# Kernel tuning notes

Measured on AMD Instinct MI355X. Metric: run time of the kernel, lower is better.

Reference implementation:

```python
import jax, jax.numpy as jnp
import numpy as np

B, N, K = 16, 8192, 16
H1, H3 = 512, 64
EPS = 1e-5


def _bn(x, g, b):
    # BatchNorm1d training-mode math: normalize per-channel (last axis) over all other axes.
    ax = tuple(range(x.ndim - 1))
    m = x.mean(ax, keepdims=True)
    v = x.var(ax, keepdims=True)  # biased variance, as in torch BN forward
    return (x - m) * jax.lax.rsqrt(v + EPS) * g + b


def _gather(h, idx):
    # h: [b,n,f], idx: [b,n,k] -> [b,n,k,f] per-batch neighbor gather
    return jax.vmap(lambda hb, ib: hb[ib])(h, idx)


def _forward(data, knn, e1_w, e1_b, e1_g, e1_be,
             gc1_w, gc1_b, g1_g, g1_be, gc2_w, gc2_b, g2_g, g2_be,
             e2_w, e2_b, e2_g, e2_be,
             d1_w, d1_b, d1_g, d1_be, d2_w, d2_b, d2_g, d2_be):
    b, n, _ = data.shape
    # local covariance features
    neigh = _gather(data, knn)                       # [b,n,K,3]
    cen = neigh - neigh.mean(axis=2, keepdims=True)
    cov = jnp.einsum('bnki,bnkj->bnij', cen, cen) / (K - 1)
    x = jnp.concatenate([data, cov.reshape(b, n, 9)], axis=-1)  # [b,n,12]
    # e_layers1: Linear(12,h3) + BN + ReLU
    x = jax.nn.relu(_bn(x @ e1_w + e1_b, e1_g, e1_be))
    # GCNConv over uniform-degree kNN graph with self loop: (h_i + sum_j h_j)/(K+1)
    deg = float(K + 1)
    h = x @ gc1_w
    h = (h + _gather(h, knn).sum(axis=2)) / deg + gc1_b
    x = jax.nn.relu(_bn(h, g1_g, g1_be))
    h = x @ gc2_w
    h = (h + _gather(h, knn).sum(axis=2)) / deg + gc2_b
    x = jax.nn.relu(_bn(h, g2_g, g2_be))             # [b,n,h1]
    # AdaptiveMaxPool1d(1) over nodes
    x = x.max(axis=1, keepdims=True)                 # [b,1,h1]
    # e_layers2: Linear(h1,h1) + BN + ReLU
    x = jax.nn.relu(_bn(x @ e2_w + e2_b, e2_g, e2_be))
    # decode: folding grid
    nx_ = int(1 + (n * 120 / 60) ** 0.5)
    ny_ = int(1 + (n * 60 / 120) ** 0.5)
    xg = jnp.linspace(1.0, 120.0, nx_)
    yg = jnp.linspace(1.0, 60.0, ny_)
    grid = jnp.stack(jnp.meshgrid(xg, yg, indexing='ij'), axis=-1).reshape(-1, 2)[:n]
    kfeat = jnp.broadcast_to(x, (b, n, x.shape[-1]))  # codeword repeated per node
    y = jnp.broadcast_to(grid[None], (b, n, 2))
    z = jnp.concatenate([kfeat, y], axis=-1)          # [b,n,h1+2]
    z = jax.nn.relu(_bn(z @ d1_w + d1_b, d1_g, d1_be))
    z = jnp.concatenate([kfeat, z], axis=-1)          # [b,n,h1+3]
    z = jax.nn.relu(_bn(z @ d2_w + d2_b, d2_g, d2_be))
    return z                                          # [b,n,3]


def setup_inputs() -> dict:
    key = jax.random.key(0)
    ks = jax.random.split(key, 8)

    def lin(k, i, o):
        s = 1.0 / np.sqrt(i)
        return jax.random.uniform(k, (i, o), jnp.float32, -s, s)

    ones = lambda c: jnp.ones((c,), jnp.float32)
    zeros = lambda c: jnp.zeros((c,), jnp.float32)
    return {
        'data': jax.random.normal(ks[0], (B, N, 3), jnp.float32),
        'knn': jax.random.randint(ks[1], (B, N, K), 0, N),
        'e1_w': lin(ks[2], 12, H3), 'e1_b': zeros(H3), 'e1_g': ones(H3), 'e1_be': zeros(H3),
        'gc1_w': lin(ks[3], H3, 2 * H3), 'gc1_b': zeros(2 * H3), 'g1_g': ones(2 * H3), 'g1_be': zeros(2 * H3),
        'gc2_w': lin(ks[4], 2 * H3, H1), 'gc2_b': zeros(H1), 'g2_g': ones(H1), 'g2_be': zeros(H1),
        'e2_w': lin(ks[5], H1, H1), 'e2_b': zeros(H1), 'e2_g': ones(H1), 'e2_be': zeros(H1),
        'd1_w': lin(ks[6], H1 + 2, 3), 'd1_b': zeros(3), 'd1_g': ones(3), 'd1_be': zeros(3),
        'd2_w': lin(ks[7], H1 + 3, 3), 'd2_b': zeros(3), 'd2_g': ones(3), 'd2_be': zeros(3),
    }


def reference(data, knn, e1_w, e1_b, e1_g, e1_be,
              gc1_w, gc1_b, g1_g, g1_be, gc2_w, gc2_b, g2_g, g2_be,
              e2_w, e2_b, e2_g, e2_be,
              d1_w, d1_b, d1_g, d1_be, d2_w, d2_b, d2_g, d2_be):
    return _forward(data, knn, e1_w, e1_b, e1_g, e1_be,
                    gc1_w, gc1_b, g1_g, g1_be, gc2_w, gc2_b, g2_g, g2_be,
                    e2_w, e2_b, e2_g, e2_be,
                    d1_w, d1_b, d1_g, d1_be, d2_w, d2_b, d2_g, d2_be)
```

## Files before the change

kernel.cpp:

```cpp
#include <hip/hip_runtime.h>
#include <hip/hip_fp16.h>
#include <stdint.h>

#define BATCH 16
#define NPTS  8192
#define KNN   16
#define NROWS (BATCH*NPTS)
#define EPSBN 1e-5f
#define DEGINV (1.0f/17.0f)

typedef _Float16 f16x8 __attribute__((ext_vector_type(8)));
typedef float    f32x4 __attribute__((ext_vector_type(4)));

__device__ __forceinline__ unsigned short f2hu(float f) {
    union { _Float16 h; unsigned short u; } cv;
    cv.h = (_Float16)f;
    return cv.u;
}
__device__ __forceinline__ float hu2f(unsigned short u) {
    union { unsigned short u; _Float16 h; } cv;
    cv.u = u;
    return (float)cv.h;
}
__device__ __forceinline__ unsigned fenc(float f) {
    unsigned u = __float_as_uint(f);
    return (int)u >= 0 ? (u | 0x80000000u) : ~u;
}
__device__ __forceinline__ float fdec(unsigned k) {
    return (k & 0x80000000u) ? __uint_as_float(k & 0x7FFFFFFFu) : __uint_as_float(~k);
}

#define SZ_S1    0
#define SZ_S2P   128
#define SZ_S3P   16512
#define SZ_S4    82048
#define SZ_C1    83072
#define SZ_GN    83080
#define SZ_D2    83088
#define SZ_SCSH1 83096
#define SZ_SCSH2 83224
#define SZ_TOT   83480

__global__ __launch_bounds__(256) void k_prep(
    const float* __restrict__ gc1w, const float* __restrict__ gc2w,
    const float* __restrict__ d1w, const float* __restrict__ d1b,
    unsigned short* __restrict__ W1T, unsigned short* __restrict__ W2T,
    float* __restrict__ gn, float* __restrict__ statszone, unsigned* __restrict__ mm)
{
    int t = blockIdx.x * 256 + threadIdx.x;
    int NT_ = gridDim.x * 256;
    for (int i = t; i < 65536; i += NT_) {
        int c = i >> 7, k = i & 127;
        W2T[i] = f2hu(gc2w[k * 512 + c]);
    }
    for (int i = t; i < 8192; i += NT_) {
        int c = i >> 6, k = i & 63;
        W1T[i] = f2hu(gc1w[k * 128 + c]);
    }
    for (int i = t; i < SZ_TOT; i += NT_) statszone[i] = 0.f;
    for (int i = t; i < 8192; i += NT_) mm[i] = 0u;
    for (int i = t; i < 8192; i += NT_) mm[8192 + i] = 0xFFFFFFFFu;
    for (int n = t; n < 8192; n += NT_) {
        int ix = n / 65, iy = n % 65;
        float gx = 1.f + ix * (119.f / 128.f);
        float gy = 1.f + iy * (59.f / 64.f);
        #pragma unroll
        for (int j = 0; j < 3; j++)
            gn[n * 3 + j] = gx * d1w[512 * 3 + j] + gy * d1w[513 * 3 + j] + d1b[j];
    }
}

__global__ __launch_bounds__(256) void k_cov_e1(
    const float* __restrict__ data, const int* __restrict__ knn,
    const float* __restrict__ e1w, const float* __restrict__ e1b,
    float* __restrict__ a1)
{
    __shared__ float w[12 * 64];
    __shared__ float bias[64];
    int tid = threadIdx.x;
    for (int i = tid; i < 768; i += 256) w[i] = e1w[i];
    if (tid < 64) bias[tid] = e1b[tid];
    __syncthreads();

    int gid = blockIdx.x * 256 + tid;
    int b = gid >> 13;
    const float* db = data + (size_t)b * NPTS * 3;
    const int4* k4 = (const int4*)knn + gid * 4;

    float sx = 0, sy = 0, sz = 0, Sxx = 0, Sxy = 0, Sxz = 0, Syy = 0, Syz = 0, Szz = 0;
    #pragma unroll
    for (int jj = 0; jj < 4; jj++) {
        int4 q = k4[jj];
        int id[4] = {q.x, q.y, q.z, q.w};
        #pragma unroll
        for (int u = 0; u < 4; u++) {
            const float* p = db + (size_t)id[u] * 3;
            float x = p[0], y = p[1], z = p[2];
            sx += x; sy += y; sz += z;
            Sxx += x * x; Sxy += x * y; Sxz += x * z;
            Syy += y * y; Syz += y * z; Szz += z * z;
        }
    }
    float mx = sx * (1.f / 16.f), my = sy * (1.f / 16.f), mz = sz * (1.f / 16.f);
    const float inv15 = 1.f / 15.f;
    float x12[12];
    x12[0] = data[(size_t)gid * 3 + 0];
    x12[1] = data[(size_t)gid * 3 + 1];
    x12[2] = data[(size_t)gid * 3 + 2];
    x12[3] = (Sxx - 16.f * mx * mx) * inv15;
    x12[4] = (Sxy - 16.f * mx * my) * inv15;
    x12[5] = (Sxz - 16.f * mx * mz) * inv15;
    x12[6] = x12[4];
    x12[7] = (Syy - 16.f * my * my) * inv15;
    x12[8] = (Syz - 16.f * my * mz) * inv15;
    x12[9] = x12[5];
    x12[10] = x12[8];
    x12[11] = (Szz - 16.f * mz * mz) * inv15;

    float* arow = a1 + (size_t)gid * 64;
    for (int c0 = 0; c0 < 64; c0 += 4) {
        float4 v;
        float* vv = (float*)&v;
        #pragma unroll
        for (int u = 0; u < 4; u++) {
            int c = c0 + u;
            float acc = bias[c];
            #pragma unroll
            for (int i = 0; i < 12; i++) acc += x12[i] * w[i * 64 + c];
            vv[u] = acc;
        }
        *(float4*)(arow + c0) = v;
    }
}

__global__ __launch_bounds__(256) void k_reduce_a1(
    const float* __restrict__ a1, float* __restrict__ stats1)
{
    int tid = threadIdx.x;
    int c = tid & 63, rq = tid >> 6;
    float s = 0.f, q = 0.f;
    for (int row = blockIdx.x * 4 + rq; row < NROWS; row += gridDim.x * 4) {
        float v = a1[(size_t)row * 64 + c];
        s += v; q += v * v;
    }
    __shared__ float red[2][256];
    red[0][tid] = s; red[1][tid] = q;
    __syncthreads();
    if (tid < 64) {
        s = red[0][tid] + red[0][tid + 64] + red[0][tid + 128] + red[0][tid + 192];
        q = red[1][tid] + red[1][tid + 64] + red[1][tid + 128] + red[1][tid + 192];
        atomicAdd(stats1 + tid, s);
        atomicAdd(stats1 + 64 + tid, q);
    }
}

template <int C, int NPARTS>
__global__ __launch_bounds__(256) void k_bncoef(
    const float* __restrict__ statsIn,
    const float* __restrict__ gamma, const float* __restrict__ beta,
    float* __restrict__ scsh)
{
    int ch = threadIdx.x;
    if (ch < C) {
        float s = 0.f, q = 0.f;
        for (int p = 0; p < NPARTS; p++) {
            s += statsIn[p * 2 * C + ch];
            q += statsIn[p * 2 * C + C + ch];
        }
        float m = s * (1.f / NROWS);
        float var = fmaxf(q * (1.f / NROWS) - m * m, 0.f);
        float sc = gamma[ch] * rsqrtf(var + EPSBN);
        scsh[ch] = sc;
        scsh[C + ch] = beta[ch] - m * sc;
    }
}

template <int CIN>
__global__ __launch_bounds__(256) void k_gather(
    const float* __restrict__ ain, const int* __restrict__ knn,
    const float* __restrict__ scsh, unsigned short* __restrict__ S)
{
    constexpr int GPR = CIN / 4;
    constexpr int R = 256 / GPR;
    constexpr int BPB = NPTS / R;

    __shared__ int nidx[R * KNN];

    int tid = threadIdx.x;
    int blk = blockIdx.x;
    int xcd = blk & 7;
    int idx = blk >> 3;
    int batch = xcd + 8 * (idx / BPB);
    int within = idx % BPB;
    int node0 = batch * NPTS + within * R;

    if (tid < R * KNN / 4) {
        const int4* ksrc = (const int4*)(knn + (size_t)node0 * KNN);
        ((int4*)nidx)[tid] = ksrc[tid];
    }
    __syncthreads();

    int t = tid & (GPR - 1);
    int r = tid / GPR;
    int col4 = t * 4;
    float4 scv = *(const float4*)(scsh + col4);
    float4 shv = *(const float4*)(scsh + CIN + col4);

    int row = node0 + r;
    const float* abase = ain + (size_t)batch * NPTS * CIN;

    float4 v = *(const float4*)(ain + (size_t)row * CIN + col4);
    float a0 = fmaxf(v.x * scv.x + shv.x, 0.f);
    float a1v = fmaxf(v.y * scv.y + shv.y, 0.f);
    float a2v = fmaxf(v.z * scv.z + shv.z, 0.f);
    float a3v = fmaxf(v.w * scv.w + shv.w, 0.f);
    #pragma unroll
    for (int jn = 0; jn < KNN; jn++) {
        int src = nidx[r * KNN + jn];
        float4 wv = *(const float4*)(abase + (size_t)src * CIN + col4);
        a0  += fmaxf(wv.x * scv.x + shv.x, 0.f);
        a1v += fmaxf(wv.y * scv.y + shv.y, 0.f);
        a2v += fmaxf(wv.z * scv.z + shv.z, 0.f);
        a3v += fmaxf(wv.w * scv.w + shv.w, 0.f);
    }
    uint2 o;
    o.x = f2hu(a0)  | ((unsigned)f2hu(a1v) << 16);
    o.y = f2hu(a2v) | ((unsigned)f2hu(a3v) << 16);
    *(uint2*)(S + (size_t)row * CIN + col4) = o;
}

template <int CIN>
__global__ __launch_bounds__(256) void k_gather16(
    const unsigned short* __restrict__ ain, const int* __restrict__ knn,
    const float* __restrict__ scsh, unsigned short* __restrict__ S)
{
    constexpr int GPR = CIN / 8;
    constexpr int R = 256 / GPR;
    constexpr int BPB = NPTS / R;

    __shared__ int nidx[R * KNN];

    int tid = threadIdx.x;
    int blk = blockIdx.x;
    int xcd = blk & 7;
    int idx = blk >> 3;
    int batch = xcd + 8 * (idx / BPB);
    int within = idx % BPB;
    int node0 = batch * NPTS + within * R;

    if (tid < R * KNN / 4) {
        const int4* ksrc = (const int4*)(knn + (size_t)node0 * KNN);
        ((int4*)nidx)[tid] = ksrc[tid];
    }
    __syncthreads();

    int t = tid & (GPR - 1);
    int r = tid / GPR;
    int col8 = t * 8;
    float sc8[8], sh8[8];
    #pragma unroll
    for (int j = 0; j < 8; j++) { sc8[j] = scsh[col8 + j]; sh8[j] = scsh[CIN + col8 + j]; }

    int row = node0 + r;
    const unsigned short* abase = ain + (size_t)batch * NPTS * CIN;

    float acc8[8];
    {
        uint4 v = *(const uint4*)(ain + (size_t)row * CIN + col8);
        unsigned wds[4] = {v.x, v.y, v.z, v.w};
        #pragma unroll
        for (int j = 0; j < 4; j++) {
            acc8[2*j]   = fmaxf(hu2f((unsigned short)(wds[j] & 0xFFFF)) * sc8[2*j]   + sh8[2*j],   0.f);
            acc8[2*j+1] = fmaxf(hu2f((unsigned short)(wds[j] >> 16))    * sc8[2*j+1] + sh8[2*j+1], 0.f);
        }
    }
    #pragma unroll
    for (int jn = 0; jn < KNN; jn++) {
        int src = nidx[r * KNN + jn];
        uint4 v = *(const uint4*)(abase + (size_t)src * CIN + col8);
        unsigned wds[4] = {v.x, v.y, v.z, v.w};
        #pragma unroll
        for (int j = 0; j < 4; j++) {
            acc8[2*j]   += fmaxf(hu2f((unsigned short)(wds[j] & 0xFFFF)) * sc8[2*j]   + sh8[2*j],   0.f);
            acc8[2*j+1] += fmaxf(hu2f((unsigned short)(wds[j] >> 16))    * sc8[2*j+1] + sh8[2*j+1], 0.f);
        }
    }
    uint4 o;
    o.x = f2hu(acc8[0]) | ((unsigned)f2hu(acc8[1]) << 16);
    o.y = f2hu(acc8[2]) | ((unsigned)f2hu(acc8[3]) << 16);
    o.z = f2hu(acc8[4]) | ((unsigned)f2hu(acc8[5]) << 16);
    o.w = f2hu(acc8[6]) | ((unsigned)f2hu(acc8[7]) << 16);
    *(uint4*)(S + (size_t)row * CIN + col8) = o;
}

template <int CIN, int COUT, bool STORE>
__global__ __launch_bounds__(256) void k_gemm(
    const unsigned short* __restrict__ S, const unsigned short* __restrict__ WT,
    const float* __restrict__ bias,
    unsigned short* __restrict__ aout, float* __restrict__ statsOut, unsigned* __restrict__ mm)
{
    constexpr int KC = CIN / 32;
    constexpr int NT = COUT / 64;
    constexpr int NHALF = (NT >= 2) ? 2 : 1;
    constexpr int NTH = NT / NHALF;
    constexpr int MT = 128;
    constexpr int BPB = NPTS / MT;

    int tid = threadIdx.x;
    int blk = blockIdx.x;
    int xcd = blk & 7;
    int idx = blk >> 3;
    int batch = xcd + 8 * (idx / BPB);
    int within = idx % BPB;
    int node0 = batch * NPTS + within * MT;
    int pout = batch * 4 + (within >> 4);

    int lane = tid & 63, wv = tid >> 6;
    int n15 = lane & 15, qd = lane >> 4;
    int c0 = wv * (COUT / 4);

    const unsigned short* Sbase = S + (size_t)node0 * CIN + (size_t)n15 * CIN + qd * 8;

    #pragma unroll
    for (int half = 0; half < NHALF; half++) {
        f16x8 wf[KC][NTH];
        float bz[NTH];
        #pragma unroll
        for (int nth = 0; nth < NTH; nth++) {
            int c = c0 + (half * NTH + nth) * 16 + n15;
            bz[nth] = bias[c];
            #pragma unroll
            for (int kc = 0; kc < KC; kc++)
                wf[kc][nth] = *(const f16x8*)(WT + (size_t)c * CIN + kc * 32 + qd * 8);
        }
        float sA[NTH], qA[NTH], mxA[NTH], mnA[NTH];
        #pragma unroll
        for (int nth = 0; nth < NTH; nth++) {
            sA[nth] = 0.f; qA[nth] = 0.f; mxA[nth] = -3.4e38f; mnA[nth] = 3.4e38f;
        }

        for (int mt = 0; mt < MT / 16; mt++) {
            f16x8 af[KC];
            #pragma unroll
            for (int kc = 0; kc < KC; kc++)
                af[kc] = *(const f16x8*)(Sbase + (size_t)mt * 16 * CIN + kc * 32);

            f32x4 acc[NTH];
            #pragma unroll
            for (int nth = 0; nth < NTH; nth++) acc[nth] = (f32x4)(0.f);
            #pragma unroll
            for (int kc = 0; kc < KC; kc++)
                #pragma unroll
                for (int nth = 0; nth < NTH; nth++)
                    acc[nth] = __builtin_amdgcn_mfma_f32_16x16x32_f16(af[kc], wf[kc][nth], acc[nth], 0, 0, 0);

            #pragma unroll
            for (int nth = 0; nth < NTH; nth++) {
                int c = c0 + (half * NTH + nth) * 16 + n15;
                #pragma unroll
                for (int r = 0; r < 4; r++) {
                    float v = acc[nth][r] * DEGINV + bz[nth];
                    if (STORE) {
                        int node = node0 + mt * 16 + qd * 4 + r;
                        aout[(size_t)node * COUT + c] = f2hu(v);
                    }
                    sA[nth] += v; qA[nth] += v * v;
                    mxA[nth] = fmaxf(mxA[nth], v); mnA[nth] = fminf(mnA[nth], v);
                }
            }
        }

        #pragma unroll
        for (int nth = 0; nth < NTH; nth++) {
            int c = c0 + (half * NTH + nth) * 16 + n15;
            float s = sA[nth], q = qA[nth];
            s += __shfl_xor(s, 16); s += __shfl_xor(s, 32);
            q += __shfl_xor(q, 16); q += __shfl_xor(q, 32);
            if (!STORE) {
                float mx = mxA[nth], mn = mnA[nth];
                mx = fmaxf(mx, __shfl_xor(mx, 16)); mx = fmaxf(mx, __shfl_xor(mx, 32));
                mn = fminf(mn, __shfl_xor(mn, 16)); mn = fminf(mn, __shfl_xor(mn, 32));
                if (lane < 16) {
                    atomicMax(mm + batch * COUT + c, fenc(mx));
                    atomicMin(mm + BATCH * COUT + batch * COUT + c, fenc(mn));
                }
            }
            if (lane < 16) {
                atomicAdd(statsOut + (size_t)pout * 2 * COUT + c, s);
                atomicAdd(statsOut + (size_t)pout * 2 * COUT + COUT + c, q);
            }
        }
    }
}

__global__ __launch_bounds__(256) void k_e2(
    const float* __restrict__ stats3p, const unsigned* __restrict__ mm,
    const float* __restrict__ g2g, const float* __restrict__ g2be,
    const float* __restrict__ e2w, const float* __restrict__ e2b,
    float* __restrict__ a4, float* __restrict__ stats4)
{
    __shared__ float pooled[512];
    int b = blockIdx.x, tid = threadIdx.x;
    for (int c = tid; c < 512; c += 256) {
        float s = 0.f, qq = 0.f;
        for (int p = 0; p < 64; p++) {
            s += stats3p[p * 1024 + c];
            qq += stats3p[p * 1024 + 512 + c];
        }
        float m = s * (1.f / NROWS);
        float var = fmaxf(qq * (1.f / NROWS) - m * m, 0.f);
        float sc = g2g[c] * rsqrtf(var + EPSBN);
        float sh = g2be[c] - m * sc;
        float amax = fdec(mm[b * 512 + c]);
        float amin = fdec(mm[8192 + b * 512 + c]);
        pooled[c] = fmaxf(fmaxf(sc * amax + sh, 0.f), fmaxf(sc * amin + sh, 0.f));
    }
    __syncthreads();
    int ca = tid, cb = tid + 256;
    float acc1 = e2b[ca], acc2 = e2b[cb];
    for (int f = 0; f < 512; f++) {
        float pv = pooled[f];
        acc1 += pv * e2w[f * 512 + ca];
        acc2 += pv * e2w[f * 512 + cb];
    }
    a4[b * 512 + ca] = acc1; a4[b * 512 + cb] = acc2;
    atomicAdd(stats4 + ca, acc1); atomicAdd(stats4 + 512 + ca, acc1 * acc1);
    atomicAdd(stats4 + cb, acc2); atomicAdd(stats4 + 512 + cb, acc2 * acc2);
}

__global__ __launch_bounds__(256) void k_code(
    const float* __restrict__ a4, const float* __restrict__ stats4,
    const float* __restrict__ e2g, const float* __restrict__ e2be,
    const float* __restrict__ d1w, const float* __restrict__ d2w,
    const float* __restrict__ gn,
    float* __restrict__ c1, float* __restrict__ c2,
    float* __restrict__ c1stats, float* __restrict__ gnstats)
{
    int b = blockIdx.x, tid = threadIdx.x;
    int lane = tid & 63, wv = tid >> 6;
    float p1[3] = {0, 0, 0}, p2[3] = {0, 0, 0};
    for (int c = tid; c < 512; c += 256) {
        float s = stats4[c], qq = stats4[512 + c];
        float m = s * (1.f / 16.f);
        float var = fmaxf(qq * (1.f / 16.f) - m * m, 0.f);
        float sc = e2g[c] * rsqrtf(var + EPSBN);
        float sh = e2be[c] - m * sc;
        float cv = fmaxf(sc * a4[b * 512 + c] + sh, 0.f);
        #pragma unroll
        for (int j = 0; j < 3; j++) {
            p1[j] += cv * d1w[c * 3 + j];
            p2[j] += cv * d2w[c * 3 + j];
        }
    }
    __shared__ float red[4][6];
    #pragma unroll
    for (int j = 0; j < 3; j++)
        for (int off = 32; off; off >>= 1) {
            p1[j] += __shfl_xor(p1[j], off);
            p2[j] += __shfl_xor(p2[j], off);
        }
    if (lane == 0) {
        #pragma unroll
        for (int j = 0; j < 3; j++) { red[wv][j] = p1[j]; red[wv][3 + j] = p2[j]; }
    }
    __syncthreads();
    if (tid < 3) {
        float v = red[0][tid] + red[1][tid] + red[2][tid] + red[3][tid];
        c1[b * 3 + tid] = v;
        atomicAdd(c1stats + tid, v);
        atomicAdd(c1stats + 3 + tid, v * v);
    } else if (tid < 6) {
        int j = tid - 3;
        float v = red[0][tid] + red[1][tid] + red[2][tid] + red[3][tid];
        c2[b * 3 + j] = v;
    }
    if (blockIdx.x == 0) {
        float g1[3] = {0, 0, 0}, g2s[3] = {0, 0, 0};
        for (int n = tid; n < NPTS; n += 256) {
            #pragma unroll
            for (int j = 0; j < 3; j++) {
                float g = gn[n * 3 + j];
                g1[j] += g; g2s[j] += g * g;
            }
        }
        #pragma unroll
        for (int j = 0; j < 3; j++)
            for (int off = 32; off; off >>= 1) {
                g1[j] += __shfl_xor(g1[j], off);
                g2s[j] += __shfl_xor(g2s[j], off);
            }
        __shared__ float redg[4][6];
        if (lane == 0) {
            #pragma unroll
            for (int j = 0; j < 3; j++) { redg[wv][j] = g1[j]; redg[wv][3 + j] = g2s[j]; }
        }
        __syncthreads();
        if (tid < 6)
            gnstats[tid] = redg[0][tid] + redg[1][tid] + redg[2][tid] + redg[3][tid];
    }
}

__device__ __forceinline__ void d1_coefs(
    const float* c1stats, const float* gnstats,
    const float* d1g, const float* d1be, float* scd, float* shd)
{
    #pragma unroll
    for (int j = 0; j < 3; j++) {
        float mc = c1stats[j] * (1.f / 16.f), qc = c1stats[3 + j] * (1.f / 16.f);
        float mg = gnstats[j] * (1.f / 8192.f), qg = gnstats[3 + j] * (1.f / 8192.f);
        float m = mc + mg;
        float var = fmaxf((qc - mc * mc) + (qg - mg * mg), 0.f);
        float sc = d1g[j] * rsqrtf(var + EPSBN);
        scd[j] = sc;
        shd[j] = d1be[j] - m * sc;
    }
}

__global__ __launch_bounds__(256) void k_d2stats(
    const float* __restrict__ c1, const float* __restrict__ c2, const float* __restrict__ gn,
    const float* __restrict__ c1stats, const float* __restrict__ gnstats,
    const float* __restrict__ d1g, const float* __restrict__ d1be,
    const float* __restrict__ d2w, const float* __restrict__ d2b,
    float* __restrict__ statsd2)
{
    int gid = blockIdx.x * 256 + threadIdx.x;
    int b = gid >> 13, n = gid & 8191;
    int lane = threadIdx.x & 63, wv = threadIdx.x >> 6;
    float scd[3], shd[3];
    d1_coefs(c1stats, gnstats, d1g, d1be, scd, shd);
    float z3[3];
    #pragma unroll
    for (int j = 0; j < 3; j++)
        z3[j] = fmaxf(scd[j] * (c1[b * 3 + j] + gn[n * 3 + j]) + shd[j], 0.f);
    float vals[6];
    #pragma unroll
    for (int u = 0; u < 3; u++) {
        float a = c2[b * 3 + u]
                + z3[0] * d2w[512 * 3 + u]
                + z3[1] * d2w[513 * 3 + u]
                + z3[2] * d2w[514 * 3 + u]
                + d2b[u];
        vals[u] = a; vals[3 + u] = a * a;
    }
    #pragma unroll
    for (int j = 0; j < 6; j++)
        for (int off = 32; off; off >>= 1) vals[j] += __shfl_xor(vals[j], off);
    __shared__ float red[4][6];
    if (lane == 0) {
        #pragma unroll
        for (int j = 0; j < 6; j++) red[wv][j] = vals[j];
    }
    __syncthreads();
    if (threadIdx.x < 6)
        atomicAdd(statsd2 + threadIdx.x,
                  red[0][threadIdx.x] + red[1][threadIdx.x] + red[2][threadIdx.x] + red[3][threadIdx.x]);
}

__global__ __launch_bounds__(256) void k_out(
    const float* __restrict__ c1, const float* __restrict__ c2, const float* __restrict__ gn,
    const float* __restrict__ c1stats, const float* __restrict__ gnstats,
    const float* __restrict__ statsd2,
    const float* __restrict__ d1g, const float* __restrict__ d1be,
    const float* __restrict__ d2w, const float* __restrict__ d2b,
    const float* __restrict__ d2g, const float* __restrict__ d2be,
    float* __restrict__ out)
{
    int gid = blockIdx.x * 256 + threadIdx.x;
    int b = gid >> 13, n = gid & 8191;
    float scd[3], shd[3];
    d1_coefs(c1stats, gnstats, d1g, d1be, scd, shd);
    float z3[3];
    #pragma unroll
    for (int j = 0; j < 3; j++)
        z3[j] = fmaxf(scd[j] * (c1[b * 3 + j] + gn[n * 3 + j]) + shd[j], 0.f);
    #pragma unroll
    for (int u = 0; u < 3; u++) {
        float a = c2[b * 3 + u]
                + z3[0] * d2w[512 * 3 + u]
                + z3[1] * d2w[513 * 3 + u]
                + z3[2] * d2w[514 * 3 + u]
                + d2b[u];
        float m2 = statsd2[u] * (1.f / (float)NROWS);
        float v2 = fmaxf(statsd2[3 + u] * (1.f / (float)NROWS) - m2 * m2, 0.f);
        float sc = d2g[u] * rsqrtf(v2 + EPSBN);
        float sh = d2be[u] - m2 * sc;
        out[(size_t)gid * 3 + u] = fmaxf(sc * a + sh, 0.f);
    }
}

extern "C" void kernel_launch(void* const* d_in, const int* in_sizes, int n_in,
                              void* d_out, int out_size, void* d_ws, size_t ws_size,
                              hipStream_t stream)
{
    (void)in_sizes; (void)n_in; (void)out_size; (void)ws_size;
    const float* data = (const float*)d_in[0];
    const int*   knn  = (const int*)d_in[1];
    const float* e1w = (const float*)d_in[2],  *e1b = (const float*)d_in[3];
    const float* e1g = (const float*)d_in[4],  *e1be = (const float*)d_in[5];
    const float* gc1w = (const float*)d_in[6], *gc1b = (const float*)d_in[7];
    const float* g1g = (const float*)d_in[8],  *g1be = (const float*)d_in[9];
    const float* gc2w = (const float*)d_in[10], *gc2b = (const float*)d_in[11];
    const float* g2g = (const float*)d_in[12], *g2be = (const float*)d_in[13];
    const float* e2w = (const float*)d_in[14], *e2b = (const float*)d_in[15];
    const float* e2g = (const float*)d_in[16], *e2be = (const float*)d_in[17];
    const float* d1w = (const float*)d_in[18], *d1b = (const float*)d_in[19];
    const float* d1g = (const float*)d_in[20], *d1be = (const float*)d_in[21];
    const float* d2w = (const float*)d_in[22], *d2b = (const float*)d_in[23];
    const float* d2g = (const float*)d_in[24], *d2be = (const float*)d_in[25];

    char* p = (char*)d_ws;
    auto alloc = [&](size_t bytes) -> void* {
        void* r = (void*)p;
        p += (bytes + 255) & ~(size_t)255;
        return r;
    };
    float* a1 = (float*)alloc((size_t)NROWS * 64 * 4);
    unsigned short* a2h = (unsigned short*)alloc((size_t)NROWS * 128 * 2);
    unsigned short* s1 = (unsigned short*)alloc((size_t)NROWS * 64 * 2);
    unsigned short* W1T = (unsigned short*)alloc(8192 * 2);
    unsigned short* W2T = (unsigned short*)alloc(65536 * 2);
    float* statszone = (float*)alloc(SZ_TOT * 4);
    float* stats1  = statszone + SZ_S1;
    float* stats2p = statszone + SZ_S2P;
    float* stats3p = statszone + SZ_S3P;
    float* stats4  = statszone + SZ_S4;
    float* c1stats = statszone + SZ_C1;
    float* gnstats = statszone + SZ_GN;
    float* statsd2 = statszone + SZ_D2;
    float* scsh1   = statszone + SZ_SCSH1;
    float* scsh2   = statszone + SZ_SCSH2;
    unsigned* mm = (unsigned*)alloc(16384 * 4);
    float* a4 = (float*)alloc(16 * 512 * 4);
    float* c1 = (float*)alloc(64 * 4);
    float* c2 = (float*)alloc(64 * 4);
    float* gn = (float*)alloc(8192 * 3 * 4);
    unsigned short* s2 = (unsigned short*)a1;

    k_prep<<<64, 256, 0, stream>>>(gc1w, gc2w, d1w, d1b, W1T, W2T, gn, statszone, mm);
    k_cov_e1<<<512, 256, 0, stream>>>(data, knn, e1w, e1b, a1);
    k_reduce_a1<<<256, 256, 0, stream>>>(a1, stats1);
    k_bncoef<64, 1><<<1, 256, 0, stream>>>(stats1, e1g, e1be, scsh1);
    k_gather<64><<<NROWS / 16, 256, 0, stream>>>(a1, knn, scsh1, s1);
    k_gemm<64, 128, true><<<1024, 256, 0, stream>>>(s1, W1T, gc1b, a2h, stats2p, nullptr);
    k_bncoef<128, 64><<<1, 256, 0, stream>>>(stats2p, g1g, g1be, scsh2);
    k_gather16<128><<<NROWS / 16, 256, 0, stream>>>(a2h, knn, scsh2, s2);
    k_gemm<128, 512, false><<<1024, 256, 0, stream>>>(s2, W2T, gc2b, nullptr, stats3p, mm);
    k_e2<<<16, 256, 0, stream>>>(stats3p, mm, g2g, g2be, e2w, e2b, a4, stats4);
    k_code<<<16, 256, 0, stream>>>(a4, stats4, e2g, e2be, d1w, d2w, gn, c1, c2, c1stats, gnstats);
    k_d2stats<<<512, 256, 0, stream>>>(c1, c2, gn, c1stats, gnstats, d1g, d1be, d2w, d2b, statsd2);
    k_out<<<512, 256, 0, stream>>>(c1, c2, gn, c1stats, gnstats, statsd2,
                                   d1g, d1be, d2w, d2b, d2g, d2be, (float*)d_out);
}
```

Baseline: 404.4 us.

## Stage GEMM A-tile in LDS, halve row tile, defer bias/scale in stats

The GEMM kernel now loads its A tile (64 rows) cooperatively into padded shared memory, so the four waves no longer each read it from global memory. The row tile is halved and the grid doubled, which raises block count and occupancy. Per-element bias and scale work in the statistics loop is removed: raw accumulator sums, squares and min/max are collected, then turned into biased statistics algebraically once per channel. The costs are an LDS footprint, a block-wide barrier, more atomics from the doubled grid, and slightly different floating-point rounding in the variance.

```diff
diff --git a/kernel.cpp b/kernel.cpp
--- a/kernel.cpp
+++ b/kernel.cpp
@@ -303,8 +303,11 @@
     constexpr int NT = COUT / 64;
     constexpr int NHALF = (NT >= 2) ? 2 : 1;
     constexpr int NTH = NT / NHALF;
-    constexpr int MT = 128;
+    constexpr int MT = 64;
+    constexpr int SST = CIN + 8;
     constexpr int BPB = NPTS / MT;
+
+    __shared__ alignas(16) unsigned short sA[MT * SST];
 
     int tid = threadIdx.x;
     int blk = blockIdx.x;
@@ -313,14 +316,24 @@
     int batch = xcd + 8 * (idx / BPB);
     int within = idx % BPB;
     int node0 = batch * NPTS + within * MT;
-    int pout = batch * 4 + (within >> 4);
+    int pout = batch * 4 + (within >> 5);
+
+    {
+        constexpr int TOT = MT * CIN / 8;
+        const uint4* src = (const uint4*)(S + (size_t)node0 * CIN);
+        #pragma unroll
+        for (int i = tid; i < TOT; i += 256) {
+            int row = i / (CIN / 8);
+            int col8 = (i % (CIN / 8)) * 8;
+            *(uint4*)&sA[row * SST + col8] = src[i];
+        }
+    }
+    __syncthreads();
 
     int lane = tid & 63, wv = tid >> 6;
     int n15 = lane & 15, qd = lane >> 4;
     int c0 = wv * (COUT / 4);
 
-    const unsigned short* Sbase = S + (size_t)node0 * CIN + (size_t)n15 * CIN + qd * 8;
-
     #pragma unroll
     for (int half = 0; half < NHALF; half++) {
         f16x8 wf[KC][NTH];
@@ -333,17 +346,18 @@
             for (int kc = 0; kc < KC; kc++)
                 wf[kc][nth] = *(const f16x8*)(WT + (size_t)c * CIN + kc * 32 + qd * 8);
         }
-        float sA[NTH], qA[NTH], mxA[NTH], mnA[NTH];
+        float sacc[NTH], qacc[NTH], mxa[NTH], mna[NTH];
         #pragma unroll
         for (int nth = 0; nth < NTH; nth++) {
-            sA[nth] = 0.f; qA[nth] = 0.f; mxA[nth] = -3.4e38f; mnA[nth] = 3.4e38f;
-        }
-
+            sacc[nth] = 0.f; qacc[nth] = 0.f; mxa[nth] = -3.4e38f; mna[nth] = 3.4e38f;
+        }
+
+        #pragma unroll
         for (int mt = 0; mt < MT / 16; mt++) {
             f16x8 af[KC];
             #pragma unroll
             for (int kc = 0; kc < KC; kc++)
-                af[kc] = *(const f16x8*)(Sbase + (size_t)mt * 16 * CIN + kc * 32);
+                af[kc] = *(const f16x8*)&sA[(mt * 16 + n15) * SST + kc * 32 + qd * 8];
 
             f32x4 acc[NTH];
             #pragma unroll
@@ -359,13 +373,18 @@
                 int c = c0 + (half * NTH + nth) * 16 + n15;
                 #pragma unroll
                 for (int r = 0; r < 4; r++) {
-                    float v = acc[nth][r] * DEGINV + bz[nth];
+                    float a = acc[nth][r];
+                    sacc[nth] += a;
+                    qacc[nth] = fmaf(a, a, qacc[nth]);
+                    if (!STORE) {
+                        mxa[nth] = fmaxf(mxa[nth], a);
+                        mna[nth] = fminf(mna[nth], a);
+                    }
                     if (STORE) {
+                        float v = a * DEGINV + bz[nth];
                         int node = node0 + mt * 16 + qd * 4 + r;
                         aout[(size_t)node * COUT + c] = f2hu(v);
                     }
-                    sA[nth] += v; qA[nth] += v * v;
-                    mxA[nth] = fmaxf(mxA[nth], v); mnA[nth] = fminf(mnA[nth], v);
                 }
             }
         }
@@ -373,19 +392,22 @@
         #pragma unroll
         for (int nth = 0; nth < NTH; nth++) {
             int c = c0 + (half * NTH + nth) * 16 + n15;
-            float s = sA[nth], q = qA[nth];
-            s += __shfl_xor(s, 16); s += __shfl_xor(s, 32);
-            q += __shfl_xor(q, 16); q += __shfl_xor(q, 32);
+            float S_ = sacc[nth], Q_ = qacc[nth];
+            S_ += __shfl_xor(S_, 16); S_ += __shfl_xor(S_, 32);
+            Q_ += __shfl_xor(Q_, 16); Q_ += __shfl_xor(Q_, 32);
             if (!STORE) {
-                float mx = mxA[nth], mn = mnA[nth];
+                float mx = mxa[nth], mn = mna[nth];
                 mx = fmaxf(mx, __shfl_xor(mx, 16)); mx = fmaxf(mx, __shfl_xor(mx, 32));
                 mn = fminf(mn, __shfl_xor(mn, 16)); mn = fminf(mn, __shfl_xor(mn, 32));
                 if (lane < 16) {
-                    atomicMax(mm + batch * COUT + c, fenc(mx));
-                    atomicMin(mm + BATCH * COUT + batch * COUT + c, fenc(mn));
+                    atomicMax(mm + batch * COUT + c, fenc(mx * DEGINV + bz[nth]));
+                    atomicMin(mm + BATCH * COUT + batch * COUT + c, fenc(mn * DEGINV + bz[nth]));
                 }
             }
             if (lane < 16) {
+                float b = bz[nth];
+                float s = DEGINV * S_ + (float)MT * b;
+                float q = DEGINV * DEGINV * Q_ + 2.f * DEGINV * b * S_ + (float)MT * b * b;
                 atomicAdd(statsOut + (size_t)pout * 2 * COUT + c, s);
                 atomicAdd(statsOut + (size_t)pout * 2 * COUT + COUT + c, q);
             }
@@ -641,10 +663,10 @@
     k_reduce_a1<<<256, 256, 0, stream>>>(a1, stats1);
     k_bncoef<64, 1><<<1, 256, 0, stream>>>(stats1, e1g, e1be, scsh1);
     k_gather<64><<<NROWS / 16, 256, 0, stream>>>(a1, knn, scsh1, s1);
-    k_gemm<64, 128, true><<<1024, 256, 0, stream>>>(s1, W1T, gc1b, a2h, stats2p, nullptr);
+    k_gemm<64, 128, true><<<2048, 256, 0, stream>>>(s1, W1T, gc1b, a2h, stats2p, nullptr);
     k_bncoef<128, 64><<<1, 256, 0, stream>>>(stats2p, g1g, g1be, scsh2);
     k_gather16<128><<<NROWS / 16, 256, 0, stream>>>(a2h, knn, scsh2, s2);
-    k_gemm<128, 512, false><<<1024, 256, 0, stream>>>(s2, W2T, gc2b, nullptr, stats3p, mm);
+    k_gemm<128, 512, false><<<2048, 256, 0, stream>>>(s2, W2T, gc2b, nullptr, stats3p, mm);
     k_e2<<<16, 256, 0, stream>>>(stats3p, mm, g2g, g2be, e2w, e2b, a4, stats4);
     k_code<<<16, 256, 0, stream>>>(a4, stats4, e2g, e2be, d1w, d2w, gn, c1, c2, c1stats, gnstats);
     k_d2stats<<<512, 256, 0, stream>>>(c1, c2, gn, c1stats, gnstats, d1g, d1be, d2w, d2b, statsd2);
```

Measured after the change: 383.2 us. 5.2% less time.
